# Kernel tuning notes

Measured on AMD Instinct MI355X. Metric: run time of the kernel, lower is better.

Reference implementation:

```python
import jax, jax.numpy as jnp
import numpy as np

E = 20    # number of residue types (rc.restypes)
NB = 2    # num_blocks per AngleHead
NA = 7    # num_angles
C_S = 384
C_H = 128
BS, L = 8, 2048


def setup_inputs() -> dict:
    key = jax.random.key(0)
    ks = jax.random.split(key, 16)
    sc = 0.02
    return {
        "s": jax.random.normal(ks[0], (BS, L, C_S), dtype=jnp.float32),
        "s_init": jax.random.normal(ks[1], (BS, L, C_S), dtype=jnp.float32),
        "aatype": jax.random.randint(ks[2], (BS, L), 0, E, dtype=jnp.int32),
        # stacked per-residue-type AngleHead params
        "Win": jax.random.normal(ks[3], (E, C_S, C_H), dtype=jnp.float32) * sc,
        "b_in": jax.random.normal(ks[4], (E, C_H), dtype=jnp.float32) * sc,
        "Winit": jax.random.normal(ks[5], (E, C_S, C_H), dtype=jnp.float32) * sc,
        "b_init2": jax.random.normal(ks[6], (E, C_H), dtype=jnp.float32) * sc,
        "Wb1": jax.random.normal(ks[7], (E, NB, C_H, C_H), dtype=jnp.float32) * sc,
        "bb1": jax.random.normal(ks[8], (E, NB, C_H), dtype=jnp.float32) * sc,
        "Wb2": jax.random.normal(ks[9], (E, NB, C_H, C_H), dtype=jnp.float32) * sc,
        "bb2": jax.random.normal(ks[10], (E, NB, C_H), dtype=jnp.float32) * sc,
        "Wout": jax.random.normal(ks[11], (E, C_H, NA * 2), dtype=jnp.float32) * sc,
        "b_out": jax.random.normal(ks[12], (E, NA * 2), dtype=jnp.float32) * sc,
    }


def reference(s, s_init, aatype, Win, b_in, Winit, b_init2, Wb1, bb1, Wb2, bb2, Wout, b_out):
    relu = jax.nn.relu
    bs, seq_len, c_s = s.shape
    N = bs * seq_len
    sf = s.reshape(N, c_s)          # [N, c_s]
    si = s_init.reshape(N, c_s)     # [N, c_s]

    # Dense dispatch: run every token through all E per-type heads, then
    # combine with the one-hot routing mask (math identical to the torch
    # gather/scatter loop over residue types).
    h = jnp.einsum('nd,edh->neh', relu(sf), Win) + b_in            # [N,E,H]
    h = h + jnp.einsum('nd,edh->neh', relu(si), Winit) + b_init2   # [N,E,H]

    for b in range(NB):  # ResidualBlock1d: s + W2 @ relu(W1 @ relu(s))
        a = jnp.einsum('neh,ehk->nek', relu(h), Wb1[:, b]) + bb1[:, b]
        a = jnp.einsum('nek,ekh->neh', relu(a), Wb2[:, b]) + bb2[:, b]
        h = h + a

    out = jnp.einsum('neh,eho->neo', relu(h), Wout) + b_out        # [N,E,2*NA]
    sel = jax.nn.one_hot(aatype.reshape(N), E, dtype=out.dtype)    # [N,E]
    ang = jnp.einsum('neo,ne->no', out, sel).reshape(bs, seq_len, NA, 2)

    # F.normalize(dim=-1): x / max(||x||, eps)
    nrm = jnp.maximum(jnp.linalg.norm(ang, axis=-1, keepdims=True), 1e-12)
    return ang / nrm
```

## Files before the change

kernel.cpp:

```cpp
#include <hip/hip_runtime.h>
#include <math.h>

#define E_TYPES 20
#define NBLK 2
#define NANG 7
#define CS 384
#define CH 128
#define N_TOK (8 * 2048)
#define TOK 16
#define TPB 256
#define TPB_MAIN 512
#define KC 128
#define MAX_TILES (N_TOK / TOK + E_TYPES)
#define NPREP 64

#define HIST_OFF 0

#define WT1_OFF (256 * 1024)
#define WT1_SZ  (20 * 8 * 24 * 2048)
#define WTR_OFF (WT1_OFF + WT1_SZ)

typedef __attribute__((ext_vector_type(8))) short bfrag;
typedef __attribute__((ext_vector_type(4))) float f32x4;
typedef unsigned short (*arr136)[136];

__device__ __forceinline__ void split_bf16(float x, unsigned short& h, unsigned short& l) {
    unsigned int u = __float_as_uint(x);
    unsigned int hb = (u + 0x7FFFu + ((u >> 16) & 1u)) & 0xFFFF0000u;
    h = (unsigned short)(hb >> 16);
    float r = x - __uint_as_float(hb);
    unsigned int v = __float_as_uint(r);
    l = (unsigned short)((v + 0x7FFFu + ((v >> 16) & 1u)) >> 16);
}

__global__ void prep1(const float* __restrict__ Win, const float* __restrict__ Winit,
                      const float* __restrict__ Wb1, const float* __restrict__ Wb2,
                      const int* __restrict__ aatype, int* __restrict__ wsI,
                      unsigned short* __restrict__ wt) {
    __shared__ int lh[E_TYPES];
    int bid = blockIdx.x;
    int t = threadIdx.x;
    if (bid >= 1600) {
        int b2 = bid - 1600;
        if (t < E_TYPES) lh[t] = 0;
        __syncthreads();
        int idx = b2 * 256 + t;
        if (idx < N_TOK) atomicAdd(&lh[aatype[idx]], 1);
        __syncthreads();
        if (t < E_TYPES) wsI[HIST_OFF + b2 * E_TYPES + t] = lh[t];
        return;
    }
    int gid = bid * 256 + t;
    unsigned short h[8], l[8];
    if (gid < 245760) {
        int lane = gid & 63;
        int bi = gid >> 6;
        int kb = bi % 24;
        int r = bi / 24;
        int nt = r & 7, e = r >> 3;
        int n = nt * 16 + (lane & 15);
        int k0 = kb * 32 + (lane >> 4) * 8;
        #pragma unroll
        for (int j = 0; j < 8; j++) {
            int k = k0 + j;
            float x = (k < CS) ? Win[((size_t)e * CS + k) * CH + n]
                               : Winit[((size_t)e * CS + (k - CS)) * CH + n];
            split_bf16(x, h[j], l[j]);
        }
        unsigned short* dst = wt + (WT1_OFF / 2) + (size_t)bi * 1024 + lane * 8;
        *(bfrag*)dst = *(bfrag*)h;
        *(bfrag*)(dst + 512) = *(bfrag*)l;
    } else {
        gid -= 245760;
        int lane = gid & 63;
        int bi = gid >> 6;
        int kb = bi & 3;
        int nt = (bi >> 2) & 7;
        int m4 = (bi >> 5) & 3;
        int e = bi >> 7;
        int b = m4 >> 1;
        const float* W = (m4 & 1) ? Wb2 : Wb1;
        int n = nt * 16 + (lane & 15);
        int k0 = kb * 32 + (lane >> 4) * 8;
        #pragma unroll
        for (int j = 0; j < 8; j++) {
            int k = k0 + j;
            float x = W[(((size_t)e * NBLK + b) * CH + k) * CH + n];
            split_bf16(x, h[j], l[j]);
        }
        unsigned short* dst = wt + (WTR_OFF / 2) + (size_t)bi * 1024 + lane * 8;
        *(bfrag*)dst = *(bfrag*)h;
        *(bfrag*)(dst + 512) = *(bfrag*)l;
    }
}

#define MFMA(a, b, c) __builtin_amdgcn_mfma_f32_16x16x32_bf16((a), (b), (c), 0, 0, 0)

__global__ __launch_bounds__(TPB_MAIN)
void angle_main(const float* __restrict__ s, const float* __restrict__ si,
                const float* __restrict__ b_in, const float* __restrict__ b_init2,
                const float* __restrict__ bb1, const float* __restrict__ bb2,
                const float* __restrict__ Wout, const float* __restrict__ b_out,
                const int* __restrict__ aatype,
                const int* __restrict__ wsI, const unsigned short* __restrict__ wt,
                float* __restrict__ out)
{
    #define BUFSZ 8704
    __shared__ __align__(16) char pool[2 * BUFSZ];
    __shared__ int ptok[TOK];
    __shared__ int cntS[E_TYPES];

    arr136 AH0 = (arr136)(pool);
    arr136 AL0 = (arr136)(pool + 4352);
    arr136 AH1 = (arr136)(pool + BUFSZ);
    arr136 AL1 = (arr136)(pool + BUFSZ + 4352);
    float (*Hf)[132] = (float (*)[132])(pool);
    float (*Of)[16]  = (float (*)[16])(pool + BUFSZ);

    int t = threadIdx.x;
    int w = t >> 6, lane = t & 63;
    int lane15 = lane & 15, quad = lane >> 4;

    int bid = blockIdx.x;
    const int q = MAX_TILES >> 3, r = MAX_TILES & 7;
    int xcd = bid & 7, sub = bid >> 3;
    int tile = (xcd < r ? xcd * (q + 1) : r * (q + 1) + (xcd - r) * q) + sub;

    if (w == 0 && lane < E_TYPES) {
        int c = 0;
        #pragma unroll
        for (int b = 0; b < NPREP; b++) c += wsI[HIST_OFF + b * E_TYPES + lane];
        cntS[lane] = c;
    }
    __syncthreads();

    int pos = tile * TOK;
    int e = -1, poff_e = 0;
    {
        int accT = 0;
        #pragma unroll
        for (int ee = 0; ee < E_TYPES; ee++) {
            int pad = (cntS[ee] + TOK - 1) & ~(TOK - 1);
            if (e < 0 && pos < accT + pad) { e = ee; poff_e = accT; }
            accT += pad;
        }
        if (pos >= accT) return;
    }
    int pos_in = pos - poff_e;
    int n = cntS[e] - pos_in; if (n > TOK) n = TOK;

    int nc = w * 16 + lane15;
    const bfrag* wt1 = (const bfrag*)((const char*)wt + WT1_OFF);
    const bfrag* wtr = (const bfrag*)((const char*)wt + WTR_OFF);
    size_t wb = (size_t)(e * 8 + w) * 24;

    bfrag Bd[2][4];
    {
        const bfrag* nb = wt1 + wb * 128 + lane;
        Bd[0][0] = nb[0];   Bd[0][1] = nb[128];
        Bd[0][2] = nb[64];  Bd[0][3] = nb[192];
    }
    float bv_in  = b_in[e * CH + nc] + b_init2[e * CH + nc];
    float bvb1a = bb1[(e * NBLK + 0) * CH + nc];
    float bvb1b = bb1[(e * NBLK + 1) * CH + nc];
    float bvb2a = bb2[(e * NBLK + 0) * CH + nc];
    float bvb2b = bb2[(e * NBLK + 1) * CH + nc];

    if (w == 0) {
        int hb = wsI[HIST_OFF + lane * E_TYPES + e];
        int inc = hb;
        #pragma unroll
        for (int d = 1; d < 64; d <<= 1) { int v = __shfl_up(inc, d); if (lane >= d) inc += v; }
        int pre = inc - hb;
        unsigned long long mle = __ballot(pre <= pos_in);
        int cb = 63 - __clzll(mle);
        int running = __shfl(pre, cb);
        int base = cb * 256;
        int lim = pos_in + n;
        while (running < lim && base < N_TOK) {
            const int4 a4 = *(const int4*)&aatype[base + lane * 4];
            int m0 = (a4.x == e), m1 = (a4.y == e), m2 = (a4.z == e), m3 = (a4.w == e);
            int c = m0 + m1 + m2 + m3;
            int incl = c;
            #pragma unroll
            for (int d = 1; d < 64; d <<= 1) { int v = __shfl_up(incl, d); if (lane >= d) incl += v; }
            int rk = running + incl - c;
            int tk = base + lane * 4;
            if (m0) { if (rk >= pos_in && rk < lim) ptok[rk - pos_in] = tk;     rk++; }
            if (m1) { if (rk >= pos_in && rk < lim) ptok[rk - pos_in] = tk + 1; rk++; }
            if (m2) { if (rk >= pos_in && rk < lim) ptok[rk - pos_in] = tk + 2; rk++; }
            if (m3) { if (rk >= pos_in && rk < lim) ptok[rk - pos_in] = tk + 3; rk++; }
            running += __shfl(incl, 63);
            base += 256;
        }
        int t0 = ptok[0];
        if (lane >= n && lane < TOK) ptok[lane] = t0;
    }
    __syncthreads();

    int srow = t >> 5;
    int scol = (t & 31) * 4;
    size_t rowoff = (size_t)ptok[srow] * CS + scol;
    float4 p0 = *(const float4*)(s + rowoff);

    f32x4 aA = (f32x4){bv_in, bv_in, bv_in, bv_in};
    f32x4 aB = (f32x4){0.f, 0.f, 0.f, 0.f};

    #pragma unroll
    for (int c = 0; c < 6; c++) {
        arr136 WAH = (c & 1) ? AH1 : AH0;
        arr136 WAL = (c & 1) ? AL1 : AL0;
        {
            ushort4 hv, lv;
            split_bf16(fmaxf(p0.x, 0.f), hv.x, lv.x);
            split_bf16(fmaxf(p0.y, 0.f), hv.y, lv.y);
            split_bf16(fmaxf(p0.z, 0.f), hv.z, lv.z);
            split_bf16(fmaxf(p0.w, 0.f), hv.w, lv.w);
            *(ushort4*)&WAH[srow][scol] = hv;
            *(ushort4*)&WAL[srow][scol] = lv;
        }
        if (c < 5) {
            const float* src = (c + 1 < 3) ? s : si;
            int kb0 = ((c + 1 < 3) ? (c + 1) : (c - 2)) * KC;
            p0 = *(const float4*)(src + rowoff + kb0);
        }
        __syncthreads();
        const bfrag* wbase = wt1 + (wb + c * 4) * 128 + lane;
        bfrag c2h = wbase[256], c2l = wbase[320];
        bfrag c3h = wbase[384], c3l = wbase[448];
        #pragma unroll
        for (int ks = 0; ks < 4; ks++) {
            bfrag bh = (ks == 0) ? Bd[c & 1][0] : (ks == 1) ? Bd[c & 1][1]
                      : (ks == 2) ? c2h : c3h;
            bfrag bl = (ks == 0) ? Bd[c & 1][2] : (ks == 1) ? Bd[c & 1][3]
                      : (ks == 2) ? c2l : c3l;
            int kl = ks * 32 + quad * 8;
            bfrag ah = *(const bfrag*)&WAH[lane15][kl];
            bfrag al = *(const bfrag*)&WAL[lane15][kl];
            aA = MFMA(ah, bh, aA);
            aB = MFMA(ah, bl, aB);
            aB = MFMA(al, bh, aB);
            if (ks == 1) {
                const bfrag* nb = (c < 5)
                    ? wt1 + (wb + (c + 1) * 4) * 128 + lane
                    : wtr + ((size_t)(e * 4 + 0) * 8 + w) * 4 * 128 + lane;
                Bd[(c + 1) & 1][0] = nb[0];   Bd[(c + 1) & 1][1] = nb[128];
                Bd[(c + 1) & 1][2] = nb[64];  Bd[(c + 1) & 1][3] = nb[192];
            }
        }
        __syncthreads();
    }

    f32x4 h0 = aA + aB;
    {
        #pragma unroll
        for (int rr = 0; rr < 4; rr++) {
            unsigned short hh, ll;
            split_bf16(fmaxf(h0[rr], 0.f), hh, ll);
            AH0[quad * 4 + rr][nc] = hh;
            AL0[quad * 4 + rr][nc] = ll;
        }
    }
    __syncthreads();

    #pragma unroll
    for (int g = 0; g < 4; g++) {
        arr136 WAH = (g & 1) ? AH1 : AH0;
        arr136 WAL = (g & 1) ? AL1 : AL0;
        const bfrag* wbase = wtr + ((size_t)(e * 4 + g) * 8 + w) * 4 * 128 + lane;
        bfrag c2h = wbase[256], c2l = wbase[320];
        bfrag c3h = wbase[384], c3l = wbase[448];
        float bv = (g & 1) ? ((g >> 1) ? bvb2b : bvb2a)
                           : ((g >> 1) ? bvb1b : bvb1a);
        f32x4 rA = (f32x4){bv, bv, bv, bv};
        f32x4 rB = (f32x4){0.f, 0.f, 0.f, 0.f};
        #pragma unroll
        for (int ks = 0; ks < 4; ks++) {
            bfrag bh = (ks == 0) ? Bd[g & 1][0] : (ks == 1) ? Bd[g & 1][1]
                      : (ks == 2) ? c2h : c3h;
            bfrag bl = (ks == 0) ? Bd[g & 1][2] : (ks == 1) ? Bd[g & 1][3]
                      : (ks == 2) ? c2l : c3l;
            int kl = ks * 32 + quad * 8;
            bfrag ah = *(const bfrag*)&WAH[lane15][kl];
            bfrag al = *(const bfrag*)&WAL[lane15][kl];
            rA = MFMA(ah, bh, rA);
            rB = MFMA(ah, bl, rB);
            rB = MFMA(al, bh, rB);
            if (ks == 1 && g < 3) {
                const bfrag* nb = wtr + ((size_t)(e * 4 + g + 1) * 8 + w) * 4 * 128 + lane;
                Bd[(g + 1) & 1][0] = nb[0];   Bd[(g + 1) & 1][1] = nb[128];
                Bd[(g + 1) & 1][2] = nb[64];  Bd[(g + 1) & 1][3] = nb[192];
            }
        }
        f32x4 r0 = rA + rB;
        if (g & 1) h0 += r0;
        if (g < 3) {
            f32x4 cur = (g & 1) ? h0 : r0;
            arr136 NH = (g & 1) ? AH0 : AH1;
            arr136 NL = (g & 1) ? AL0 : AL1;
            #pragma unroll
            for (int rr = 0; rr < 4; rr++) {
                unsigned short hh, ll;
                split_bf16(fmaxf(cur[rr], 0.f), hh, ll);
                NH[quad * 4 + rr][nc] = hh;
                NL[quad * 4 + rr][nc] = ll;
            }
            __syncthreads();
        } else {
            #pragma unroll
            for (int rr = 0; rr < 4; rr++)
                Hf[quad * 4 + rr][nc] = fmaxf(h0[rr], 0.f);
            __syncthreads();
        }
    }

    const float* WoutE = Wout + (size_t)e * CH * (NANG * 2);
    const float* boutE = b_out + (size_t)e * (NANG * 2);
    for (int idx = t; idx < n * (NANG * 2); idx += TPB_MAIN) {
        int i = idx / (NANG * 2);
        int o = idx - i * (NANG * 2);
        float v0 = boutE[o], v1 = 0.f, v2 = 0.f, v3 = 0.f;
        #pragma unroll 4
        for (int k = 0; k < CH; k += 4) {
            v0 = fmaf(Hf[i][k],     WoutE[(size_t)k * (NANG * 2) + o],       v0);
            v1 = fmaf(Hf[i][k + 1], WoutE[(size_t)(k + 1) * (NANG * 2) + o], v1);
            v2 = fmaf(Hf[i][k + 2], WoutE[(size_t)(k + 2) * (NANG * 2) + o], v2);
            v3 = fmaf(Hf[i][k + 3], WoutE[(size_t)(k + 3) * (NANG * 2) + o], v3);
        }
        Of[i][o] = (v0 + v1) + (v2 + v3);
    }
    __syncthreads();

    for (int idx = t; idx < n * NANG; idx += TPB_MAIN) {
        int i = idx / NANG;
        int a = idx - i * NANG;
        float x = Of[i][2 * a];
        float y = Of[i][2 * a + 1];
        float nr = fmaxf(sqrtf(x * x + y * y), 1e-12f);
        size_t base = (size_t)ptok[i] * (NANG * 2) + 2 * a;
        out[base]     = x / nr;
        out[base + 1] = y / nr;
    }
}

extern "C" void kernel_launch(void* const* d_in, const int* in_sizes, int n_in,
                              void* d_out, int out_size, void* d_ws, size_t ws_size,
                              hipStream_t stream) {
    const float* s       = (const float*)d_in[0];
    const float* s_init  = (const float*)d_in[1];
    const int*   aatype  = (const int*)d_in[2];
    const float* Win     = (const float*)d_in[3];
    const float* b_in    = (const float*)d_in[4];
    const float* Winit   = (const float*)d_in[5];
    const float* b_init2 = (const float*)d_in[6];
    const float* Wb1     = (const float*)d_in[7];
    const float* bb1     = (const float*)d_in[8];
    const float* Wb2     = (const float*)d_in[9];
    const float* bb2     = (const float*)d_in[10];
    const float* Wout    = (const float*)d_in[11];
    const float* b_out   = (const float*)d_in[12];
    int* wsI = (int*)d_ws;
    unsigned short* wt = (unsigned short*)d_ws;
    float* out = (float*)d_out;

    hipLaunchKernelGGL(prep1, dim3(1664), dim3(256), 0, stream,
                       Win, Winit, Wb1, Wb2, aatype, wsI, wt);
    hipLaunchKernelGGL(angle_main, dim3(MAX_TILES), dim3(TPB_MAIN), 0, stream,
                       s, s_init, b_in, b_init2, bb1, bb2, Wout, b_out,
                       aatype, wsI, wt, out);
}
```

Baseline: 159.4 us.

## Grow token tile to 64 rows so each weight fragment feeds four MFMAs

The token tile per block grows from 16 to 64 rows. Each wave now loads a full set of weight fragments per K-chunk and reuses it across four 16-row MFMA sub-tiles, which cuts global weight traffic per token by four. The residual-block loop is unrolled by hand with register double buffering of the weight fragments. The cost is four times the LDS (about 68 KB), more accumulator registers, and more padding waste per residue type. Removing the middle barrier inside the input-projection loop may also introduce a race on the double-buffered LDS.

```diff
diff --git a/kernel.cpp b/kernel.cpp
--- a/kernel.cpp
+++ b/kernel.cpp
@@ -7,8 +7,7 @@
 #define CS 384
 #define CH 128
 #define N_TOK (8 * 2048)
-#define TOK 16
-#define TPB 256
+#define TOK 64
 #define TPB_MAIN 512
 #define KC 128
 #define MAX_TILES (N_TOK / TOK + E_TYPES)
@@ -96,7 +95,60 @@
 
 #define MFMA(a, b, c) __builtin_amdgcn_mfma_f32_16x16x32_bf16((a), (b), (c), 0, 0, 0)
 
-__global__ __launch_bounds__(TPB_MAIN)
+#define LOADW(DST, BASEPTR) do {                                   \
+    const bfrag* _p = (BASEPTR);                                   \
+    DST[0] = _p[0];   DST[1] = _p[128];                            \
+    DST[2] = _p[256]; DST[3] = _p[384];                            \
+    DST[4] = _p[64];  DST[5] = _p[192];                            \
+    DST[6] = _p[320]; DST[7] = _p[448];                            \
+} while (0)
+
+#define MFMA_STAGE(WAH, WAL, CUR, AA, BB) do {                     \
+    _Pragma("unroll")                                              \
+    for (int ks = 0; ks < 4; ks++) {                               \
+        int kl = ks * 32 + quad * 8;                               \
+        _Pragma("unroll")                                          \
+        for (int m = 0; m < 4; m++) {                              \
+            bfrag ah = *(const bfrag*)&WAH[m * 16 + lane15][kl];   \
+            bfrag al = *(const bfrag*)&WAL[m * 16 + lane15][kl];   \
+            AA[m] = MFMA(ah, CUR[ks], AA[m]);                      \
+            BB[m] = MFMA(ah, CUR[4 + ks], BB[m]);                  \
+            BB[m] = MFMA(al, CUR[ks], BB[m]);                      \
+        }                                                          \
+    }                                                              \
+} while (0)
+
+#define WRITE_A(WAH, WAL) do {                                     \
+    float xv[16] = {p0.x, p0.y, p0.z, p0.w, p1.x, p1.y, p1.z, p1.w,\
+                    p2.x, p2.y, p2.z, p2.w, p3.x, p3.y, p3.z, p3.w};\
+    unsigned short h8[8], l8[8];                                   \
+    _Pragma("unroll")                                              \
+    for (int j = 0; j < 8; j++)                                    \
+        split_bf16(fmaxf(xv[j], 0.f), h8[j], l8[j]);               \
+    *(bfrag*)&WAH[srow][scol] = *(bfrag*)h8;                       \
+    *(bfrag*)&WAL[srow][scol] = *(bfrag*)l8;                       \
+    _Pragma("unroll")                                              \
+    for (int j = 0; j < 8; j++)                                    \
+        split_bf16(fmaxf(xv[8 + j], 0.f), h8[j], l8[j]);           \
+    *(bfrag*)&WAH[srow][scol + 8] = *(bfrag*)h8;                   \
+    *(bfrag*)&WAL[srow][scol + 8] = *(bfrag*)l8;                   \
+} while (0)
+
+#define WRITE_H(WAH, WAL, SRC) do {                                \
+    _Pragma("unroll")                                              \
+    for (int m = 0; m < 4; m++)                                    \
+    {                                                              \
+        _Pragma("unroll")                                          \
+        for (int rr = 0; rr < 4; rr++) {                           \
+            unsigned short hh, ll;                                 \
+            split_bf16(fmaxf(SRC[m][rr], 0.f), hh, ll);            \
+            WAH[m * 16 + quad * 4 + rr][nc] = hh;                  \
+            WAL[m * 16 + quad * 4 + rr][nc] = ll;                  \
+        }                                                          \
+    }                                                              \
+} while (0)
+
+__global__ __launch_bounds__(TPB_MAIN, 2)
 void angle_main(const float* __restrict__ s, const float* __restrict__ si,
                 const float* __restrict__ b_in, const float* __restrict__ b_init2,
                 const float* __restrict__ bb1, const float* __restrict__ bb2,
@@ -105,17 +157,17 @@
                 const int* __restrict__ wsI, const unsigned short* __restrict__ wt,
                 float* __restrict__ out)
 {
-    #define BUFSZ 8704
-    __shared__ __align__(16) char pool[2 * BUFSZ];
+    #define ABUF 17408
+    __shared__ __align__(16) char pool[4 * ABUF];
     __shared__ int ptok[TOK];
     __shared__ int cntS[E_TYPES];
 
     arr136 AH0 = (arr136)(pool);
-    arr136 AL0 = (arr136)(pool + 4352);
-    arr136 AH1 = (arr136)(pool + BUFSZ);
-    arr136 AL1 = (arr136)(pool + BUFSZ + 4352);
+    arr136 AL0 = (arr136)(pool + ABUF);
+    arr136 AH1 = (arr136)(pool + 2 * ABUF);
+    arr136 AL1 = (arr136)(pool + 3 * ABUF);
     float (*Hf)[132] = (float (*)[132])(pool);
-    float (*Of)[16]  = (float (*)[16])(pool + BUFSZ);
+    float (*Of)[16]  = (float (*)[16])(pool + 2 * ABUF);
 
     int t = threadIdx.x;
     int w = t >> 6, lane = t & 63;
@@ -154,13 +206,9 @@
     const bfrag* wtr = (const bfrag*)((const char*)wt + WTR_OFF);
     size_t wb = (size_t)(e * 8 + w) * 24;
 
-    bfrag Bd[2][4];
-    {
-        const bfrag* nb = wt1 + wb * 128 + lane;
-        Bd[0][0] = nb[0];   Bd[0][1] = nb[128];
-        Bd[0][2] = nb[64];  Bd[0][3] = nb[192];
-    }
-    float bv_in  = b_in[e * CH + nc] + b_init2[e * CH + nc];
+    bfrag Wr0[8], Wr1[8];
+    LOADW(Wr0, wt1 + wb * 128 + lane);
+    float bv_in = b_in[e * CH + nc] + b_init2[e * CH + nc];
     float bvb1a = bb1[(e * NBLK + 0) * CH + nc];
     float bvb1b = bb1[(e * NBLK + 1) * CH + nc];
     float bvb2a = bb2[(e * NBLK + 0) * CH + nc];
@@ -194,125 +242,108 @@
             base += 256;
         }
         int t0 = ptok[0];
-        if (lane >= n && lane < TOK) ptok[lane] = t0;
-    }
-    __syncthreads();
-
-    int srow = t >> 5;
-    int scol = (t & 31) * 4;
+        if (lane >= n) ptok[lane] = t0;
+    }
+    __syncthreads();
+
+    int srow = t >> 3;
+    int scol = (t & 7) * 16;
     size_t rowoff = (size_t)ptok[srow] * CS + scol;
     float4 p0 = *(const float4*)(s + rowoff);
-
-    f32x4 aA = (f32x4){bv_in, bv_in, bv_in, bv_in};
-    f32x4 aB = (f32x4){0.f, 0.f, 0.f, 0.f};
+    float4 p1 = *(const float4*)(s + rowoff + 4);
+    float4 p2 = *(const float4*)(s + rowoff + 8);
+    float4 p3 = *(const float4*)(s + rowoff + 12);
+
+    f32x4 aA[4], aB[4];
+    #pragma unroll
+    for (int m = 0; m < 4; m++) {
+        aA[m] = (f32x4){bv_in, bv_in, bv_in, bv_in};
+        aB[m] = (f32x4){0.f, 0.f, 0.f, 0.f};
+    }
 
     #pragma unroll
     for (int c = 0; c < 6; c++) {
-        arr136 WAH = (c & 1) ? AH1 : AH0;
-        arr136 WAL = (c & 1) ? AL1 : AL0;
-        {
-            ushort4 hv, lv;
-            split_bf16(fmaxf(p0.x, 0.f), hv.x, lv.x);
-            split_bf16(fmaxf(p0.y, 0.f), hv.y, lv.y);
-            split_bf16(fmaxf(p0.z, 0.f), hv.z, lv.z);
-            split_bf16(fmaxf(p0.w, 0.f), hv.w, lv.w);
-            *(ushort4*)&WAH[srow][scol] = hv;
-            *(ushort4*)&WAL[srow][scol] = lv;
-        }
+        if ((c & 1) == 0) WRITE_A(AH0, AL0);
+        else              WRITE_A(AH1, AL1);
         if (c < 5) {
             const float* src = (c + 1 < 3) ? s : si;
             int kb0 = ((c + 1 < 3) ? (c + 1) : (c - 2)) * KC;
             p0 = *(const float4*)(src + rowoff + kb0);
+            p1 = *(const float4*)(src + rowoff + kb0 + 4);
+            p2 = *(const float4*)(src + rowoff + kb0 + 8);
+            p3 = *(const float4*)(src + rowoff + kb0 + 12);
         }
         __syncthreads();
-        const bfrag* wbase = wt1 + (wb + c * 4) * 128 + lane;
-        bfrag c2h = wbase[256], c2l = wbase[320];
-        bfrag c3h = wbase[384], c3l = wbase[448];
-        #pragma unroll
-        for (int ks = 0; ks < 4; ks++) {
-            bfrag bh = (ks == 0) ? Bd[c & 1][0] : (ks == 1) ? Bd[c & 1][1]
-                      : (ks == 2) ? c2h : c3h;
-            bfrag bl = (ks == 0) ? Bd[c & 1][2] : (ks == 1) ? Bd[c & 1][3]
-                      : (ks == 2) ? c2l : c3l;
-            int kl = ks * 32 + quad * 8;
-            bfrag ah = *(const bfrag*)&WAH[lane15][kl];
-            bfrag al = *(const bfrag*)&WAL[lane15][kl];
-            aA = MFMA(ah, bh, aA);
-            aB = MFMA(ah, bl, aB);
-            aB = MFMA(al, bh, aB);
-            if (ks == 1) {
-                const bfrag* nb = (c < 5)
-                    ? wt1 + (wb + (c + 1) * 4) * 128 + lane
-                    : wtr + ((size_t)(e * 4 + 0) * 8 + w) * 4 * 128 + lane;
-                Bd[(c + 1) & 1][0] = nb[0];   Bd[(c + 1) & 1][1] = nb[128];
-                Bd[(c + 1) & 1][2] = nb[64];  Bd[(c + 1) & 1][3] = nb[192];
-            }
-        }
-        __syncthreads();
-    }
-
-    f32x4 h0 = aA + aB;
+        if ((c & 1) == 0) {
+            if (c < 5) LOADW(Wr1, wt1 + (wb + (c + 1) * 4) * 128 + lane);
+            MFMA_STAGE(AH0, AL0, Wr0, aA, aB);
+        } else {
+            if (c == 5) LOADW(Wr0, wtr + (((size_t)(e * 4) * 8 + w) * 4) * 128 + lane);
+            else        LOADW(Wr0, wt1 + (wb + (c + 1) * 4) * 128 + lane);
+            MFMA_STAGE(AH1, AL1, Wr1, aA, aB);
+        }
+    }
+
+    f32x4 h[4];
+    #pragma unroll
+    for (int m = 0; m < 4; m++) h[m] = aA[m] + aB[m];
+    WRITE_H(AH0, AL0, h);
+    __syncthreads();
+
+    f32x4 rA[4], rB[4];
+    #pragma unroll
+    for (int m = 0; m < 4; m++) {
+        rA[m] = (f32x4){bvb1a, bvb1a, bvb1a, bvb1a};
+        rB[m] = (f32x4){0.f, 0.f, 0.f, 0.f};
+    }
+    LOADW(Wr1, wtr + (((size_t)(e * 4 + 1) * 8 + w) * 4) * 128 + lane);
+    MFMA_STAGE(AH0, AL0, Wr0, rA, rB);
+    #pragma unroll
+    for (int m = 0; m < 4; m++) rA[m] += rB[m];
+    WRITE_H(AH1, AL1, rA);
+    __syncthreads();
+
+    #pragma unroll
+    for (int m = 0; m < 4; m++) {
+        rA[m] = (f32x4){bvb2a, bvb2a, bvb2a, bvb2a};
+        rB[m] = (f32x4){0.f, 0.f, 0.f, 0.f};
+    }
+    LOADW(Wr0, wtr + (((size_t)(e * 4 + 2) * 8 + w) * 4) * 128 + lane);
+    MFMA_STAGE(AH1, AL1, Wr1, rA, rB);
+    #pragma unroll
+    for (int m = 0; m < 4; m++) h[m] += rA[m] + rB[m];
+    WRITE_H(AH0, AL0, h);
+    __syncthreads();
+
+    #pragma unroll
+    for (int m = 0; m < 4; m++) {
+        rA[m] = (f32x4){bvb1b, bvb1b, bvb1b, bvb1b};
+        rB[m] = (f32x4){0.f, 0.f, 0.f, 0.f};
+    }
+    LOADW(Wr1, wtr + (((size_t)(e * 4 + 3) * 8 + w) * 4) * 128 + lane);
+    MFMA_STAGE(AH0, AL0, Wr0, rA, rB);
+    #pragma unroll
+    for (int m = 0; m < 4; m++) rA[m] += rB[m];
+    WRITE_H(AH1, AL1, rA);
+    __syncthreads();
+
+    #pragma unroll
+    for (int m = 0; m < 4; m++) {
+        rA[m] = (f32x4){bvb2b, bvb2b, bvb2b, bvb2b};
+        rB[m] = (f32x4){0.f, 0.f, 0.f, 0.f};
+    }
+    MFMA_STAGE(AH1, AL1, Wr1, rA, rB);
+    #pragma unroll
+    for (int m = 0; m < 4; m++) h[m] += rA[m] + rB[m];
+
+    #pragma unroll
+    for (int m = 0; m < 4; m++)
     {
         #pragma unroll
-        for (int rr = 0; rr < 4; rr++) {
-            unsigned short hh, ll;
-            split_bf16(fmaxf(h0[rr], 0.f), hh, ll);
-            AH0[quad * 4 + rr][nc] = hh;
-            AL0[quad * 4 + rr][nc] = ll;
-        }
-    }
-    __syncthreads();
-
-    #pragma unroll
-    for (int g = 0; g < 4; g++) {
-        arr136 WAH = (g & 1) ? AH1 : AH0;
-        arr136 WAL = (g & 1) ? AL1 : AL0;
-        const bfrag* wbase = wtr + ((size_t)(e * 4 + g) * 8 + w) * 4 * 128 + lane;
-        bfrag c2h = wbase[256], c2l = wbase[320];
-        bfrag c3h = wbase[384], c3l = wbase[448];
-        float bv = (g & 1) ? ((g >> 1) ? bvb2b : bvb2a)
-                           : ((g >> 1) ? bvb1b : bvb1a);
-        f32x4 rA = (f32x4){bv, bv, bv, bv};
-        f32x4 rB = (f32x4){0.f, 0.f, 0.f, 0.f};
-        #pragma unroll
-        for (int ks = 0; ks < 4; ks++) {
-            bfrag bh = (ks == 0) ? Bd[g & 1][0] : (ks == 1) ? Bd[g & 1][1]
-                      : (ks == 2) ? c2h : c3h;
-            bfrag bl = (ks == 0) ? Bd[g & 1][2] : (ks == 1) ? Bd[g & 1][3]
-                      : (ks == 2) ? c2l : c3l;
-            int kl = ks * 32 + quad * 8;
-            bfrag ah = *(const bfrag*)&WAH[lane15][kl];
-            bfrag al = *(const bfrag*)&WAL[lane15][kl];
-            rA = MFMA(ah, bh, rA);
-            rB = MFMA(ah, bl, rB);
-            rB = MFMA(al, bh, rB);
-            if (ks == 1 && g < 3) {
-                const bfrag* nb = wtr + ((size_t)(e * 4 + g + 1) * 8 + w) * 4 * 128 + lane;
-                Bd[(g + 1) & 1][0] = nb[0];   Bd[(g + 1) & 1][1] = nb[128];
-                Bd[(g + 1) & 1][2] = nb[64];  Bd[(g + 1) & 1][3] = nb[192];
-            }
-        }
-        f32x4 r0 = rA + rB;
-        if (g & 1) h0 += r0;
-        if (g < 3) {
-            f32x4 cur = (g & 1) ? h0 : r0;
-            arr136 NH = (g & 1) ? AH0 : AH1;
-            arr136 NL = (g & 1) ? AL0 : AL1;
-            #pragma unroll
-            for (int rr = 0; rr < 4; rr++) {
-                unsigned short hh, ll;
-                split_bf16(fmaxf(cur[rr], 0.f), hh, ll);
-                NH[quad * 4 + rr][nc] = hh;
-                NL[quad * 4 + rr][nc] = ll;
-            }
-            __syncthreads();
-        } else {
-            #pragma unroll
-            for (int rr = 0; rr < 4; rr++)
-                Hf[quad * 4 + rr][nc] = fmaxf(h0[rr], 0.f);
-            __syncthreads();
-        }
-    }
+        for (int rr = 0; rr < 4; rr++)
+            Hf[m * 16 + quad * 4 + rr][nc] = fmaxf(h[m][rr], 0.f);
+    }
+    __syncthreads();
 
     const float* WoutE = Wout + (size_t)e * CH * (NANG * 2);
     const float* boutE = b_out + (size_t)e * (NANG * 2);
```

After: 165.2 us. 3.7% more time.
